# Kernel tuning notes

Measured on AMD Instinct MI355X. Metric: run time of the kernel, lower is better.

## Reference

```python
import jax, jax.numpy as jnp
import numpy as np

N_NODES = 100000
N_EDGES = 6400000


def setup_inputs() -> dict:
    key = jax.random.key(0)
    k1, k2, k3, k4, k5, k6 = jax.random.split(key, 6)
    edge_predictions = jax.random.normal(k1, (N_EDGES,), dtype=jnp.float32)
    node_predictions = jax.random.normal(k2, (N_NODES,), dtype=jnp.float32)
    x = jax.random.uniform(k3, (N_NODES, 4), dtype=jnp.float32)  # col 2 = demand
    capacity = jnp.ones((1,), dtype=jnp.float32) * 50.0  # vehicle capacity
    y_edges = (jax.random.uniform(k4, (N_EDGES,)) < 0.1).astype(jnp.float32)
    y_nodes = jax.random.normal(k5, (N_NODES,), dtype=jnp.float32)
    edge_index = jax.random.randint(k6, (2, N_EDGES), 0, N_NODES, dtype=jnp.int64)
    return {
        'edge_predictions': edge_predictions,
        'node_predictions': node_predictions,
        'x': x,
        'capacity': capacity,
        'y_edges': y_edges,
        'y_nodes': y_nodes,
        'edge_index': edge_index,
        'num_nodes': N_NODES,
    }


def _bce_with_logits(logits, targets):
    # numerically stable elementwise BCE-with-logits
    return jnp.maximum(logits, 0.0) - logits * targets + jnp.log1p(jnp.exp(-jnp.abs(logits)))


def _focal_loss(logits, targets, alpha=0.25, gamma=2.0):
    bce = _bce_with_logits(logits, targets)
    probs = jax.nn.sigmoid(logits)
    p_t = probs * targets + (1.0 - probs) * (1.0 - targets)
    alpha_t = alpha * targets + (1.0 - alpha) * (1.0 - targets)
    return jnp.mean(alpha_t * (1.0 - p_t) ** gamma * bce)


def reference(edge_predictions, node_predictions, x, capacity, y_edges, y_nodes,
              edge_index, num_nodes):
    edge_probs = jax.nn.sigmoid(edge_predictions)
    src, dst = edge_index[0], edge_index[1]

    # single segment-sum pass over edges replaces the O(num_nodes * num_edges) loops
    in_sums = jax.ops.segment_sum(edge_probs, dst, num_segments=num_nodes)   # [N]
    out_sums = jax.ops.segment_sum(edge_probs, src, num_segments=num_nodes)  # [N]

    # coverage loss: customer nodes (1..N-1) should have in/out degree-prob == 1
    coverage = (jnp.sum((in_sums[1:] - 1.0) ** 2) + jnp.sum((out_sums[1:] - 1.0) ** 2)) \
               / (2.0 * max(num_nodes - 1, 1))

    # tour formation: flow conservation over ALL nodes
    tour_formation = jnp.sum((in_sums - out_sums) ** 2) / num_nodes

    # depot balance
    depot_balance = (in_sums[0] - out_sums[0]) ** 2

    # capacity tours: depot out-degree ~ ceil(total_demand / capacity)
    demands = x[:, 2]
    total_demand = jnp.sum(demands[1:])
    cap_value = jax.lax.stop_gradient(jnp.mean(capacity))  # torch uses .item()
    expected_tours = jnp.ceil(total_demand / cap_value)
    capacity_tours = (out_sums[0] - expected_tours) ** 2

    # similarity (focal) loss on raw logits
    similarity = _focal_loss(edge_predictions, y_edges, alpha=0.25, gamma=2.0)

    # masked node MSE (mask is data-dependent -> where-based mean)
    mask = (y_nodes >= 0.0).astype(node_predictions.dtype)
    cnt = jnp.maximum(jnp.sum(mask), 1.0)
    node_loss = jnp.sum(mask * (node_predictions - y_nodes) ** 2) / cnt

    total = (coverage * 5.0 + tour_formation * 3.0 + depot_balance * 2.0 +
             capacity_tours * 1.5 + similarity * 0.3 + node_loss * 0.1)
    return total
```

## Files before the change

### kernel.cpp

```cpp
#include <hip/hip_runtime.h>
#include <math.h>

#define RANGE_LOG 8
#define RANGE 256
#define NB_META 512
#define CAP 34400u
#define EDGES_PER_CHUNK 4096
#define SCAT_THREADS 512
#define EPT 8
#define PARTS 4



__device__ __forceinline__ float wave_reduce_sum(float v) {
    #pragma unroll
    for (int o = 32; o > 0; o >>= 1) v += __shfl_down(v, o, 64);
    return v;
}

template <int NW>
__device__ float block_reduce_sum(float v) {
    __shared__ float s[NW];
    __syncthreads();
    const int lane = threadIdx.x & 63;
    const int wid  = threadIdx.x >> 6;
    v = wave_reduce_sum(v);
    if (lane == 0) s[wid] = v;
    __syncthreads();
    float r = 0.f;
    if (wid == 0) {
        float x = (lane < NW) ? s[lane] : 0.f;
        r = wave_reduce_sum(x);
    }
    return r;
}

#define LOG2E 1.44269504f
#define LN2   0.69314718f

__device__ __forceinline__ float fast_focal(float x, float t, float& p) {
    const float ax = fabsf(x);
    const float e  = __builtin_amdgcn_exp2f(-ax * LOG2E);
    const float r  = __builtin_amdgcn_rcpf(1.f + e);
    p = (x >= 0.f) ? r : 1.f - r;
    const float sp  = __builtin_amdgcn_logf(1.f + e) * LN2;
    const float bce = fmaxf(x, 0.f) - x * t + sp;
    const float p_t = p * t + (1.f - p) * (1.f - t);
    const float a_t = 0.25f * t + 0.75f * (1.f - t);
    const float om  = 1.f - p_t;
    return a_t * om * om * bce;
}


__global__ __launch_bounds__(SCAT_THREADS, 8)
void scatter_kernel(const float* __restrict__ ep,
                    const float* __restrict__ ye,
                    const int*   __restrict__ ei,
                    unsigned* __restrict__ cursor,
                    unsigned short* __restrict__ pairs,
                    float* __restrict__ acc,
                    int E) {
    __shared__ unsigned s_hist[NB_META];
    __shared__ unsigned s_cur[NB_META];
    __shared__ unsigned s_gbase[NB_META];
    __shared__ unsigned s_pack[2 * EDGES_PER_CHUNK];

    const int tid   = threadIdx.x;
    const int lane  = tid & 63;
    const int wid   = tid >> 6;
    const int ebase = blockIdx.x * EDGES_PER_CHUNK;
    const int ec    = min(EDGES_PER_CHUNK, E - ebase);
    const int cnt   = 2 * ec;

    s_hist[tid] = 0u;
    __syncthreads();

    unsigned pk[2 * EPT];
    float local = 0.f;
    const int  le0  = tid * EPT;
    const bool full = (le0 + EPT) <= ec;

    if (full) {
        const int e0 = ebase + le0;
        #pragma unroll
        for (int h = 0; h < 2; ++h) {
            const float4 xv = *(const float4*)(ep + e0 + 4 * h);
            const float4 tv = *(const float4*)(ye + e0 + 4 * h);
            const int4   sv = *(const int4*)(ei + e0 + 4 * h);
            const int4   dv = *(const int4*)(ei + E + e0 + 4 * h);
            const float xx[4] = {xv.x, xv.y, xv.z, xv.w};
            const float tt[4] = {tv.x, tv.y, tv.z, tv.w};
            const unsigned ss[4] = {(unsigned)sv.x, (unsigned)sv.y, (unsigned)sv.z, (unsigned)sv.w};
            const unsigned dd[4] = {(unsigned)dv.x, (unsigned)dv.y, (unsigned)dv.z, (unsigned)dv.w};
            #pragma unroll
            for (int j = 0; j < 4; ++j) {
                float p;
                local += fast_focal(xx[j], tt[j], p);
                const unsigned pq = min((unsigned)(p * 128.f + 0.5f), 127u);
                const int k = 4 * h + j;
                const unsigned sb = ss[j] >> RANGE_LOG, db = dd[j] >> RANGE_LOG;
                pk[2 * k]     = (sb << 16) | ((ss[j] & (RANGE - 1)) << 8) | pq;
                pk[2 * k + 1] = (db << 16) | ((dd[j] & (RANGE - 1)) << 8) | 128u | pq;
                atomicAdd(&s_hist[sb], 1u);
                atomicAdd(&s_hist[db], 1u);
            }
        }
    } else {
        #pragma unroll
        for (int k = 0; k < EPT; ++k) {
            pk[2 * k] = 0xFFFFFFFFu;
            pk[2 * k + 1] = 0xFFFFFFFFu;
            const int el = le0 + k;
            if (el < ec) {
                const int e = ebase + el;
                float p;
                local += fast_focal(ep[e], ye[e], p);
                const unsigned pq = min((unsigned)(p * 128.f + 0.5f), 127u);
                const unsigned s = (unsigned)ei[e];
                const unsigned d = (unsigned)ei[E + e];
                const unsigned sb = s >> RANGE_LOG, db = d >> RANGE_LOG;
                pk[2 * k]     = (sb << 16) | ((s & (RANGE - 1)) << 8) | pq;
                pk[2 * k + 1] = (db << 16) | ((d & (RANGE - 1)) << 8) | 128u | pq;
                atomicAdd(&s_hist[sb], 1u);
                atomicAdd(&s_hist[db], 1u);
            }
        }
    }
    __syncthreads();

    const unsigned h = s_hist[tid];
    unsigned v = h;
    #pragma unroll
    for (int o = 1; o < 64; o <<= 1) {
        const unsigned t = (unsigned)__shfl_up((int)v, o, 64);
        if (lane >= o) v += t;
    }
    if (lane == 63) s_gbase[wid] = v;
    __syncthreads();
    if (wid == 0 && lane < 8) {
        unsigned x = s_gbase[lane];
        #pragma unroll
        for (int o = 1; o < 8; o <<= 1) {
            const unsigned t = (unsigned)__shfl_up((int)x, o, 8);
            if (lane >= o) x += t;
        }
        s_gbase[lane] = x;
    }
    __syncthreads();
    const unsigned wbase = (wid > 0) ? s_gbase[wid - 1] : 0u;
    __syncthreads();
    const unsigned excl = wbase + v - h;
    s_cur[tid]   = excl;
    s_gbase[tid] = h ? (atomicAdd(&cursor[tid], h) - excl) : 0u;
    __syncthreads();

    if (full) {
        #pragma unroll
        for (int k = 0; k < 2 * EPT; ++k) {
            const unsigned pv = pk[k];
            const unsigned r = atomicAdd(&s_cur[pv >> 16], 1u);
            s_pack[r] = pv;
        }
    } else {
        #pragma unroll
        for (int k = 0; k < 2 * EPT; ++k) {
            const unsigned pv = pk[k];
            if (pv != 0xFFFFFFFFu) {
                const unsigned r = atomicAdd(&s_cur[pv >> 16], 1u);
                s_pack[r] = pv;
            }
        }
    }
    __syncthreads();

    for (int idx = tid; idx < cnt; idx += SCAT_THREADS) {
        const unsigned pv = s_pack[idx];
        const unsigned b  = pv >> 16;
        pairs[(size_t)b * CAP + (unsigned)(s_gbase[b] + (unsigned)idx)] =
            (unsigned short)pv;
    }

    const float bs = block_reduce_sum<SCAT_THREADS / 64>(local);
    if (tid == 0) atomicAdd(&acc[0], bs);
}

__global__ __launch_bounds__(256, 8)
void accum_kernel(const unsigned* __restrict__ cursor,
                  const unsigned short* __restrict__ pairs,
                  unsigned* __restrict__ partials,
                  int N, int nbuck) {
    __shared__ unsigned sAcc[2 * RANGE];
    const int tid  = threadIdx.x;
    const int b    = blockIdx.x % nbuck;
    const int part = blockIdx.x / nbuck;
    sAcc[tid] = 0u; sAcc[tid + 256] = 0u;
    __syncthreads();

    unsigned fill = cursor[b];
    if (fill > CAP) fill = CAP;
    const unsigned lo = ((unsigned)(((unsigned long long)fill * part) / PARTS)) & ~7u;
    const unsigned hi = (part == PARTS - 1)
        ? fill
        : (((unsigned)(((unsigned long long)fill * (part + 1)) / PARTS)) & ~7u);
    const size_t gb = (size_t)b * CAP;
    const unsigned hiv = lo + ((hi - lo) & ~7u);

    for (unsigned i = lo + 8 * tid; i < hiv; i += 8 * 256) {
        const uint4 v = *(const uint4*)(pairs + gb + i);
        const unsigned d0 = v.x, d1 = v.y, d2 = v.z, d3 = v.w;
        atomicAdd(&sAcc[(d0 & 0xFFFFu) >> 7], d0 & 127u);
        atomicAdd(&sAcc[(d0 >> 23)], (d0 >> 16) & 127u);
        atomicAdd(&sAcc[(d1 & 0xFFFFu) >> 7], d1 & 127u);
        atomicAdd(&sAcc[(d1 >> 23)], (d1 >> 16) & 127u);
        atomicAdd(&sAcc[(d2 & 0xFFFFu) >> 7], d2 & 127u);
        atomicAdd(&sAcc[(d2 >> 23)], (d2 >> 16) & 127u);
        atomicAdd(&sAcc[(d3 & 0xFFFFu) >> 7], d3 & 127u);
        atomicAdd(&sAcc[(d3 >> 23)], (d3 >> 16) & 127u);
    }
    for (unsigned i = hiv + tid; i < hi; i += 256) {
        const unsigned u = pairs[gb + i];
        atomicAdd(&sAcc[u >> 7], u & 127u);
    }
    __syncthreads();

    const int nodes = min(RANGE, N - b * RANGE);
    unsigned* dstp = partials + (size_t)part * 2 * N + 2 * (size_t)(b * RANGE);
    for (int i = tid; i < nodes; i += 256) {
        *(uint2*)(dstp + 2 * i) = *(const uint2*)(&sAcc[2 * i]);
    }
}

__global__ void node_cov3_kernel(const float* __restrict__ npred,
                                 const float* __restrict__ yn,
                                 const float* __restrict__ x,
                                 const unsigned* __restrict__ partials,
                                 float* __restrict__ acc,
                                 const float* __restrict__ capacity,
                                 float* __restrict__ out,
                                 unsigned* __restrict__ done,
                                 int N, int E) {
    __shared__ bool is_last;
    const int i = blockIdx.x * blockDim.x + threadIdx.x;
    float dem = 0.f, cntm = 0.f, sq = 0.f, cov = 0.f, tour = 0.f;
    if (i < N) {
        unsigned ou = 0u, iu = 0u;
        #pragma unroll
        for (int p = 0; p < PARTS; ++p) {
            const uint2 v = *(const uint2*)(partials + (size_t)p * 2 * N + 2 * (size_t)i);
            ou += v.x;
            iu += v.y;
        }
        const float outv = (float)ou * (1.f / 128.f);
        const float inv  = (float)iu * (1.f / 128.f);
        if (i >= 1) dem = x[i * 4 + 2];
        const float y = yn[i];
        if (y >= 0.f) {
            cntm = 1.f;
            const float d = npred[i] - y;
            sq = d * d;
        }
        const float dd = inv - outv;
        tour = dd * dd;
        if (i >= 1) cov = (inv - 1.f) * (inv - 1.f) + (outv - 1.f) * (outv - 1.f);
        if (i == 0) { atomicAdd(&acc[6], inv); atomicAdd(&acc[7], outv); }
    }
    float r;
    r = block_reduce_sum<4>(dem);  if (threadIdx.x == 0) atomicAdd(&acc[1], r);
    r = block_reduce_sum<4>(cntm); if (threadIdx.x == 0) atomicAdd(&acc[2], r);
    r = block_reduce_sum<4>(sq);   if (threadIdx.x == 0) atomicAdd(&acc[3], r);
    r = block_reduce_sum<4>(cov);  if (threadIdx.x == 0) atomicAdd(&acc[4], r);
    r = block_reduce_sum<4>(tour); if (threadIdx.x == 0) atomicAdd(&acc[5], r);

    if (threadIdx.x == 0) {
        __threadfence();
        const unsigned t = atomicAdd(done, 1u);
        is_last = (t == (unsigned)(gridDim.x - 1));
    }
    __syncthreads();
    if (is_last && threadIdx.x == 0) {
        __threadfence();
        const float coverage = acc[4] / (2.0f * (float)(N - 1));
        const float tourv    = acc[5] / (float)N;
        const float in0  = acc[6];
        const float out0 = acc[7];
        const float depot = (in0 - out0) * (in0 - out0);
        const float cap = capacity[0];
        const float expected = ceilf(acc[1] / cap);
        const float cap_t = (out0 - expected) * (out0 - expected);
        const float sim = acc[0] / (float)E;
        const float node_loss = acc[3] / fmaxf(acc[2], 1.f);
        out[0] = coverage * 5.f + tourv * 3.f + depot * 2.f + cap_t * 1.5f +
                 sim * 0.3f + node_loss * 0.1f;
    }
}


__global__ void edge_kernel(const float* __restrict__ ep,
                            const float* __restrict__ ye,
                            const int*   __restrict__ src,
                            const int*   __restrict__ dst,
                            float* __restrict__ in_sums,
                            float* __restrict__ out_sums,
                            float* __restrict__ acc,
                            int E) {
    float local = 0.f;
    for (int i = blockIdx.x * blockDim.x + threadIdx.x; i < E;
         i += gridDim.x * blockDim.x) {
        const float x = ep[i];
        float p;
        local += fast_focal(x, ye[i], p);
        unsafeAtomicAdd(&out_sums[src[i]], p);
        unsafeAtomicAdd(&in_sums[dst[i]], p);
    }
    const float bs = block_reduce_sum<4>(local);
    if (threadIdx.x == 0) atomicAdd(&acc[0], bs);
}

__global__ void node_cov_kernel(const float* __restrict__ npred,
                                const float* __restrict__ yn,
                                const float* __restrict__ x,
                                const float* __restrict__ in_sums,
                                const float* __restrict__ out_sums,
                                float* __restrict__ acc,
                                const float* __restrict__ capacity,
                                float* __restrict__ out,
                                unsigned* __restrict__ done,
                                int N, int E) {
    __shared__ bool is_last;
    const int i = blockIdx.x * blockDim.x + threadIdx.x;
    float dem = 0.f, cntm = 0.f, sq = 0.f, cov = 0.f, tour = 0.f;
    if (i < N) {
        if (i >= 1) dem = x[i * 4 + 2];
        const float y = yn[i];
        if (y >= 0.f) {
            cntm = 1.f;
            const float d = npred[i] - y;
            sq = d * d;
        }
        const float a = in_sums[i];
        const float b = out_sums[i];
        const float dd = a - b;
        tour = dd * dd;
        if (i >= 1) cov = (a - 1.f) * (a - 1.f) + (b - 1.f) * (b - 1.f);
        if (i == 0) { atomicAdd(&acc[6], a); atomicAdd(&acc[7], b); }
    }
    float r;
    r = block_reduce_sum<4>(dem);  if (threadIdx.x == 0) atomicAdd(&acc[1], r);
    r = block_reduce_sum<4>(cntm); if (threadIdx.x == 0) atomicAdd(&acc[2], r);
    r = block_reduce_sum<4>(sq);   if (threadIdx.x == 0) atomicAdd(&acc[3], r);
    r = block_reduce_sum<4>(cov);  if (threadIdx.x == 0) atomicAdd(&acc[4], r);
    r = block_reduce_sum<4>(tour); if (threadIdx.x == 0) atomicAdd(&acc[5], r);

    if (threadIdx.x == 0) {
        __threadfence();
        const unsigned t = atomicAdd(done, 1u);
        is_last = (t == (unsigned)(gridDim.x - 1));
    }
    __syncthreads();
    if (is_last && threadIdx.x == 0) {
        __threadfence();
        const float coverage = acc[4] / (2.0f * (float)(N - 1));
        const float tourv    = acc[5] / (float)N;
        const float depot = (acc[6] - acc[7]) * (acc[6] - acc[7]);
        const float expected = ceilf(acc[1] / capacity[0]);
        const float cap_t = (acc[7] - expected) * (acc[7] - expected);
        const float sim = acc[0] / (float)E;
        const float node_loss = acc[3] / fmaxf(acc[2], 1.f);
        out[0] = coverage * 5.f + tourv * 3.f + depot * 2.f + cap_t * 1.5f +
                 sim * 0.3f + node_loss * 0.1f;
    }
}


extern "C" void kernel_launch(void* const* d_in, const int* in_sizes, int n_in,
                              void* d_out, int out_size, void* d_ws, size_t ws_size,
                              hipStream_t stream) {
    const float* ep       = (const float*)d_in[0];
    const float* npred    = (const float*)d_in[1];
    const float* x        = (const float*)d_in[2];
    const float* capacity = (const float*)d_in[3];
    const float* ye       = (const float*)d_in[4];
    const float* yn       = (const float*)d_in[5];
    const int*   ei       = (const int*)d_in[6];

    const int E = in_sizes[0];
    const int N = in_sizes[1];
    const int nbuck = (N + RANGE - 1) / RANGE;

    char* w = (char*)d_ws;
    float*    acc    = (float*)w;
    unsigned* cursor = (unsigned*)(w + 256);
    unsigned* done   = (unsigned*)(w + 3840);
    unsigned* partials = (unsigned*)(w + 4096);
    size_t off_pairs = 4096 + (size_t)PARTS * 2 * N * sizeof(unsigned);
    off_pairs = (off_pairs + 255) & ~(size_t)255;
    unsigned short* pairs = (unsigned short*)(w + off_pairs);
    const size_t need = off_pairs + (size_t)nbuck * CAP * sizeof(unsigned short) + 65536;

    if (nbuck <= NB_META && ws_size >= need && (E % 4) == 0 && N < (1 << 17)) {
        hipMemsetAsync(d_ws, 0, 4096, stream);
        const int nchunks = (E + EDGES_PER_CHUNK - 1) / EDGES_PER_CHUNK;
        scatter_kernel<<<nchunks, SCAT_THREADS, 0, stream>>>(
            ep, ye, ei, cursor, pairs, acc, E);
        accum_kernel<<<nbuck * PARTS, 256, 0, stream>>>(
            cursor, pairs, partials, N, nbuck);
        node_cov3_kernel<<<(N + 255) / 256, 256, 0, stream>>>(
            npred, yn, x, partials, acc, capacity, (float*)d_out, done, N, E);
    } else {
        float* in_sums  = (float*)(w + 4096);
        float* out_sums = in_sums + N;
        hipMemsetAsync(d_ws, 0, 4096 + (size_t)2 * N * sizeof(float), stream);
        edge_kernel<<<4096, 256, 0, stream>>>(ep, ye, ei, ei + E, in_sums,
                                              out_sums, acc, E);
        node_cov_kernel<<<(N + 255) / 256, 256, 0, stream>>>(
            npred, yn, x, in_sums, out_sums, acc, capacity, (float*)d_out,
            done, N, E);
    }
}
```

Measured before the change: 194.9 us.

## Reuse histogram atomic ranks for scatter; split LDS accumulators by thread parity

```diff
diff --git a/kernel.cpp b/kernel.cpp
--- a/kernel.cpp
+++ b/kernel.cpp
@@ -61,7 +61,7 @@
                     float* __restrict__ acc,
                     int E) {
     __shared__ unsigned s_hist[NB_META];
-    __shared__ unsigned s_cur[NB_META];
+    __shared__ unsigned s_off[NB_META];
     __shared__ unsigned s_gbase[NB_META];
     __shared__ unsigned s_pack[2 * EDGES_PER_CHUNK];
 
@@ -76,6 +76,7 @@
     __syncthreads();
 
     unsigned pk[2 * EPT];
+    unsigned rkp[EPT];
     float local = 0.f;
     const int  le0  = tid * EPT;
     const bool full = (le0 + EPT) <= ec;
@@ -101,8 +102,9 @@
                 const unsigned sb = ss[j] >> RANGE_LOG, db = dd[j] >> RANGE_LOG;
                 pk[2 * k]     = (sb << 16) | ((ss[j] & (RANGE - 1)) << 8) | pq;
                 pk[2 * k + 1] = (db << 16) | ((dd[j] & (RANGE - 1)) << 8) | 128u | pq;
-                atomicAdd(&s_hist[sb], 1u);
-                atomicAdd(&s_hist[db], 1u);
+                const unsigned r0 = atomicAdd(&s_hist[sb], 1u);
+                const unsigned r1 = atomicAdd(&s_hist[db], 1u);
+                rkp[k] = r0 | (r1 << 16);
             }
         }
     } else {
@@ -110,6 +112,7 @@
         for (int k = 0; k < EPT; ++k) {
             pk[2 * k] = 0xFFFFFFFFu;
             pk[2 * k + 1] = 0xFFFFFFFFu;
+            rkp[k] = 0u;
             const int el = le0 + k;
             if (el < ec) {
                 const int e = ebase + el;
@@ -121,8 +124,9 @@
                 const unsigned sb = s >> RANGE_LOG, db = d >> RANGE_LOG;
                 pk[2 * k]     = (sb << 16) | ((s & (RANGE - 1)) << 8) | pq;
                 pk[2 * k + 1] = (db << 16) | ((d & (RANGE - 1)) << 8) | 128u | pq;
-                atomicAdd(&s_hist[sb], 1u);
-                atomicAdd(&s_hist[db], 1u);
+                const unsigned r0 = atomicAdd(&s_hist[sb], 1u);
+                const unsigned r1 = atomicAdd(&s_hist[db], 1u);
+                rkp[k] = r0 | (r1 << 16);
             }
         }
     }
@@ -150,7 +154,7 @@
     const unsigned wbase = (wid > 0) ? s_gbase[wid - 1] : 0u;
     __syncthreads();
     const unsigned excl = wbase + v - h;
-    s_cur[tid]   = excl;
+    s_off[tid]   = excl;
     s_gbase[tid] = h ? (atomicAdd(&cursor[tid], h) - excl) : 0u;
     __syncthreads();
 
@@ -158,16 +162,16 @@
         #pragma unroll
         for (int k = 0; k < 2 * EPT; ++k) {
             const unsigned pv = pk[k];
-            const unsigned r = atomicAdd(&s_cur[pv >> 16], 1u);
-            s_pack[r] = pv;
+            const unsigned r  = (rkp[k >> 1] >> ((k & 1) * 16)) & 0xFFFFu;
+            s_pack[s_off[pv >> 16] + r] = pv;
         }
     } else {
         #pragma unroll
         for (int k = 0; k < 2 * EPT; ++k) {
             const unsigned pv = pk[k];
             if (pv != 0xFFFFFFFFu) {
-                const unsigned r = atomicAdd(&s_cur[pv >> 16], 1u);
-                s_pack[r] = pv;
+                const unsigned r = (rkp[k >> 1] >> ((k & 1) * 16)) & 0xFFFFu;
+                s_pack[s_off[pv >> 16] + r] = pv;
             }
         }
     }
@@ -189,11 +193,13 @@
                   const unsigned short* __restrict__ pairs,
                   unsigned* __restrict__ partials,
                   int N, int nbuck) {
-    __shared__ unsigned sAcc[2 * RANGE];
+    __shared__ unsigned sAcc[4 * RANGE];
     const int tid  = threadIdx.x;
+    const int par  = tid & 1;
     const int b    = blockIdx.x % nbuck;
     const int part = blockIdx.x / nbuck;
-    sAcc[tid] = 0u; sAcc[tid + 256] = 0u;
+    #pragma unroll
+    for (int i = 0; i < 4; ++i) sAcc[tid + 256 * i] = 0u;
     __syncthreads();
 
     unsigned fill = cursor[b];
@@ -208,25 +214,28 @@
     for (unsigned i = lo + 8 * tid; i < hiv; i += 8 * 256) {
         const uint4 v = *(const uint4*)(pairs + gb + i);
         const unsigned d0 = v.x, d1 = v.y, d2 = v.z, d3 = v.w;
-        atomicAdd(&sAcc[(d0 & 0xFFFFu) >> 7], d0 & 127u);
-        atomicAdd(&sAcc[(d0 >> 23)], (d0 >> 16) & 127u);
-        atomicAdd(&sAcc[(d1 & 0xFFFFu) >> 7], d1 & 127u);
-        atomicAdd(&sAcc[(d1 >> 23)], (d1 >> 16) & 127u);
-        atomicAdd(&sAcc[(d2 & 0xFFFFu) >> 7], d2 & 127u);
-        atomicAdd(&sAcc[(d2 >> 23)], (d2 >> 16) & 127u);
-        atomicAdd(&sAcc[(d3 & 0xFFFFu) >> 7], d3 & 127u);
-        atomicAdd(&sAcc[(d3 >> 23)], (d3 >> 16) & 127u);
+        atomicAdd(&sAcc[((((d0 & 0xFFFFu) >> 7) << 1) | par)], d0 & 127u);
+        atomicAdd(&sAcc[(((d0 >> 23) << 1) | par)], (d0 >> 16) & 127u);
+        atomicAdd(&sAcc[((((d1 & 0xFFFFu) >> 7) << 1) | par)], d1 & 127u);
+        atomicAdd(&sAcc[(((d1 >> 23) << 1) | par)], (d1 >> 16) & 127u);
+        atomicAdd(&sAcc[((((d2 & 0xFFFFu) >> 7) << 1) | par)], d2 & 127u);
+        atomicAdd(&sAcc[(((d2 >> 23) << 1) | par)], (d2 >> 16) & 127u);
+        atomicAdd(&sAcc[((((d3 & 0xFFFFu) >> 7) << 1) | par)], d3 & 127u);
+        atomicAdd(&sAcc[(((d3 >> 23) << 1) | par)], (d3 >> 16) & 127u);
     }
     for (unsigned i = hiv + tid; i < hi; i += 256) {
         const unsigned u = pairs[gb + i];
-        atomicAdd(&sAcc[u >> 7], u & 127u);
+        atomicAdd(&sAcc[(((u >> 7) << 1) | par)], u & 127u);
     }
     __syncthreads();
 
     const int nodes = min(RANGE, N - b * RANGE);
     unsigned* dstp = partials + (size_t)part * 2 * N + 2 * (size_t)(b * RANGE);
     for (int i = tid; i < nodes; i += 256) {
-        *(uint2*)(dstp + 2 * i) = *(const uint2*)(&sAcc[2 * i]);
+        const unsigned outv = sAcc[(i << 2)] + sAcc[(i << 2) | 1];
+        const unsigned inv  = sAcc[(i << 2) | 2] + sAcc[(i << 2) | 3];
+        uint2 w; w.x = outv; w.y = inv;
+        *(uint2*)(dstp + 2 * i) = w;
     }
 }
 
```

Result: no change. 194.3 us (-0.3%).
